# Optimization experiments

Hardware: AMD Instinct MI355X
Metric: run time of the kernel (lower is better)

Reference implementation:

```python
import jax, jax.numpy as jnp
import numpy as np

V = 25000
E = 100000
NODE_IN = 74
EDGE_IN = 12
OUT = 64
EHID = 128
NUM_STEPS = 6


def setup_inputs() -> dict:
    key = jax.random.key(0)
    ks = jax.random.split(key, 12)
    s = 0.05
    node_feats = jax.random.normal(ks[0], (V, NODE_IN), dtype=jnp.float32)
    edge_feats = jax.random.normal(ks[1], (E, EDGE_IN), dtype=jnp.float32)
    src = jax.random.randint(ks[2], (E,), 0, V)
    dst = jax.random.randint(ks[3], (E,), 0, V)
    # project_node_feats: Linear(node_in, out)
    Wp = jax.random.normal(ks[4], (NODE_IN, OUT), dtype=jnp.float32) * s
    bp = jnp.zeros((OUT,), dtype=jnp.float32)
    # edge network: Linear(edge_in, ehid) -> ReLU -> Linear(ehid, out*out)
    We1 = jax.random.normal(ks[5], (EDGE_IN, EHID), dtype=jnp.float32) * s
    be1 = jnp.zeros((EHID,), dtype=jnp.float32)
    We2 = jax.random.normal(ks[6], (EHID, OUT * OUT), dtype=jnp.float32) * s
    be2 = jnp.zeros((OUT * OUT,), dtype=jnp.float32)
    # NNConv output bias
    bias = jnp.zeros((OUT,), dtype=jnp.float32)
    return {
        "node_feats": node_feats, "edge_feats": edge_feats,
        "src": src, "dst": dst,
        "Wp": Wp, "bp": bp,
        "We1": We1, "be1": be1, "We2": We2, "be2": be2,
        "bias": bias,
    }


def reference(node_feats, edge_feats, src, dst, Wp, bp, We1, be1, We2, be2, bias):
    # project node features
    h = jax.nn.relu(node_feats @ Wp + bp)  # [V, OUT]
    # per-edge weight matrices (same every step -> hoist out of loop)
    ew = jax.nn.relu(edge_feats @ We1 + be1) @ We2 + be2  # [E, OUT*OUT]
    ew = ew.reshape(E, OUT, OUT)
    for _ in range(NUM_STEPS):
        # gather src node feats, batched matvec, scatter-sum to dst
        msg = jnp.einsum('ei,eio->eo', h[src], ew)  # [E, OUT]
        agg = jax.ops.segment_sum(msg, dst, num_segments=V)  # [V, OUT]
        h = jax.nn.relu(agg + bias)
    return h
```

## Files before the change

### kernel.cpp

```cpp
#include <hip/hip_runtime.h>
#include <hip/hip_bf16.h>

#define Vn 25000
#define En 100000
#define NODE_IN 74
#define EDGE_IN 12
#define OUTD 64
#define EHID 128
#define NUM_STEPS 6

#define HPAD 68

typedef __attribute__((ext_vector_type(8))) _Float16 half8;
typedef __attribute__((ext_vector_type(4))) float floatx4;

__global__ void proj_kernel(const float* __restrict__ node,
                            const float* __restrict__ Wp,
                            const float* __restrict__ bp,
                            float* __restrict__ h) {
  __shared__ float nf[NODE_IN];
  int v = blockIdx.x;
  int o = threadIdx.x;
  for (int i = o; i < NODE_IN; i += 64) nf[i] = node[(size_t)v * NODE_IN + i];
  __syncthreads();
  float acc = bp[o];
  for (int i = 0; i < NODE_IN; ++i) acc = fmaf(nf[i], Wp[i * OUTD + o], acc);
  h[(size_t)v * OUTD + o] = fmaxf(acc, 0.0f);
}

__global__ void edge_kernel(const float* __restrict__ ef,
                            const float* __restrict__ We1,
                            const float* __restrict__ be1,
                            _Float16* __restrict__ f) {
  __shared__ float es[EDGE_IN];
  int e = blockIdx.x;
  int k = threadIdx.x;
  if (k < EDGE_IN) es[k] = ef[(size_t)e * EDGE_IN + k];
  __syncthreads();
  float acc = be1[k];
  for (int j = 0; j < EDGE_IN; ++j) acc = fmaf(es[j], We1[j * EHID + k], acc);
  f[(size_t)e * EHID + k] = (_Float16)fmaxf(acc, 0.0f);
}

__global__ void w2r_kernel(const float* __restrict__ We2,
                           _Float16* __restrict__ w2s) {
  int g = blockIdx.x * 256 + threadIdx.x;
  int j = g & 7;
  int quad = (g >> 3) & 3;
  int l15 = (g >> 5) & 15;
  int c = (g >> 9) & 3;
  int step = g >> 11;
  int s = step & 3;
  int i = step >> 2;
  int k = s * 32 + quad * 8 + j;
  int col = i * 64 + c * 16 + l15;
  int eidx = g & 2047;
  int estore = eidx ^ (((eidx >> 6) & 3) << 3);
  w2s[((size_t)step << 11) | estore] = (_Float16)We2[(size_t)k * (OUTD * OUTD) + col];
}

#define GLOAD_LDS(gp, lp)                                                     \
  __builtin_amdgcn_global_load_lds(                                           \
      (const __attribute__((address_space(1))) void*)(gp),                    \
      (__attribute__((address_space(3))) void*)(lp), 16, 0, 0)

__global__ __launch_bounds__(256, 2) void msg_kernel(
    const float* __restrict__ h,
    const _Float16* __restrict__ f,
    const _Float16* __restrict__ w2s,
    const int* __restrict__ src,
    const int* __restrict__ dst,
    const float* __restrict__ be2,
    float* __restrict__ agg) {
  __shared__ __align__(16) char smem_raw[41472];
  __shared__ int s_dst[64];

  _Float16* h16 = (_Float16*)smem_raw;

  const int tid = threadIdx.x;
  const int wv = tid >> 6;
  const int lane = tid & 63;
  const int quad = lane >> 4;
  const int l15 = lane & 15;
  const int e0 = blockIdx.x * 64;

  if (tid < 64) {
    int e = e0 + tid;
    s_dst[tid] = (e < En) ? dst[e] : -1;
  }
  {
    int e = tid & 63;
    int ib = tid >> 6;
    int eg = e0 + e;
    int sv = (eg < En) ? src[eg] : 0;
    const float4* hp = reinterpret_cast<const float4*>(h + (size_t)sv * OUTD + ib * 16);
    for (int c = 0; c < 4; ++c) {
      float4 val = hp[c];
      int i4 = ib * 16 + c * 4;
      h16[(i4 + 0) * HPAD + e] = (_Float16)val.x;
      h16[(i4 + 1) * HPAD + e] = (_Float16)val.y;
      h16[(i4 + 2) * HPAD + e] = (_Float16)val.z;
      h16[(i4 + 3) * HPAD + e] = (_Float16)val.w;
    }
  }
  __syncthreads();

  half8 afr[4][4];
#pragma unroll
  for (int t = 0; t < 4; ++t) {
    int e = e0 + t * 16 + l15;
    if (e >= En) e = En - 1;
    const _Float16* fr = f + (size_t)e * EHID + quad * 8;
#pragma unroll
    for (int s = 0; s < 4; ++s)
      afr[t][s] = *reinterpret_cast<const half8*>(fr + s * 32);
  }

  floatx4 acc[4][4];
  const floatx4 zero4 = (floatx4){0.f, 0.f, 0.f, 0.f};
#pragma unroll
  for (int t = 0; t < 4; ++t)
#pragma unroll
    for (int c = 0; c < 4; ++c) acc[t][c] = zero4;

  const int ibase = wv * 16;

  char* ring = smem_raw + 8704 + wv * 8192;
  const char* w2b = (const char*)w2s;
  const int roff = l15 * 64 + ((quad ^ ((l15 >> 1) & 3)) << 4);
  const char* slot0p = ring + roff;
  const char* slot1p = ring + 4096 + roff;

#define STAGE(GS, SLOT)                                                       \
  {                                                                           \
    const char* gp_ = w2b + (size_t)(GS) * 4096 + lane * 16;                  \
    char* lp_ = ring + (SLOT) * 4096;                                         \
    GLOAD_LDS(gp_, lp_);                                                      \
    GLOAD_LDS(gp_ + 1024, lp_ + 1024);                                        \
    GLOAD_LDS(gp_ + 2048, lp_ + 2048);                                        \
    GLOAD_LDS(gp_ + 3072, lp_ + 3072);                                        \
  }

#define VM4 asm volatile("s_waitcnt vmcnt(4)" ::: "memory")
#define VM0 asm volatile("s_waitcnt vmcnt(0)" ::: "memory")
#define LGKM0 asm volatile("s_waitcnt lgkmcnt(0)" ::: "memory")
#define LGKM4 asm volatile("s_waitcnt lgkmcnt(4)" ::: "memory")
#define SB __builtin_amdgcn_sched_barrier(0)

#define KSTEP(SS, BCUR, BNXT, STSLOT, GST, LW, VW, DO_STAGE, DO_READ, RDP)    \
  {                                                                           \
    LW;                                                                       \
    SB;                                                                       \
    if (DO_STAGE) STAGE(GST, STSLOT);                                         \
    VW;                                                                       \
    if (DO_READ) {                                                            \
      BNXT[0] = *reinterpret_cast<const half8*>(RDP);                         \
      BNXT[1] = *reinterpret_cast<const half8*>(RDP + 1024);                  \
      BNXT[2] = *reinterpret_cast<const half8*>(RDP + 2048);                  \
      BNXT[3] = *reinterpret_cast<const half8*>(RDP + 3072);                  \
    }                                                                         \
    _Pragma("unroll") for (int t = 0; t < 4; ++t) {                           \
      half8 as = afr[t][SS] * hb[t];                                          \
      acc[t][0] = __builtin_amdgcn_mfma_f32_16x16x32_f16(as, BCUR[0], acc[t][0], 0, 0, 0); \
      acc[t][1] = __builtin_amdgcn_mfma_f32_16x16x32_f16(as, BCUR[1], acc[t][1], 0, 0, 0); \
      acc[t][2] = __builtin_amdgcn_mfma_f32_16x16x32_f16(as, BCUR[2], acc[t][2], 0, 0, 0); \
      acc[t][3] = __builtin_amdgcn_mfma_f32_16x16x32_f16(as, BCUR[3], acc[t][3], 0, 0, 0); \
    }                                                                         \
    SB;                                                                       \
  }

#define BUILD_HB(IV)                                                          \
  half8 hb[4];                                                                \
  _Pragma("unroll") for (int t = 0; t < 4; ++t) {                             \
    _Float16 hf = h16[(IV) * HPAD + t * 16 + l15];                            \
    hb[t] = (half8){hf, hf, hf, hf, hf, hf, hf, hf};                          \
  }

  STAGE(ibase * 4, 0);
  STAGE(ibase * 4 + 1, 1);
  VM4;
  half8 bE[4], bO[4];
  bE[0] = *reinterpret_cast<const half8*>(slot0p);
  bE[1] = *reinterpret_cast<const half8*>(slot0p + 1024);
  bE[2] = *reinterpret_cast<const half8*>(slot0p + 2048);
  bE[3] = *reinterpret_cast<const half8*>(slot0p + 3072);

  for (int ii = 0; ii < 15; ++ii) {
    int iv = ibase + ii;
    int gs = iv * 4;
    BUILD_HB(iv);
    KSTEP(0, bE, bO, 0, gs + 2, LGKM4, VM4, 1, 1, slot1p);
    KSTEP(1, bO, bE, 1, gs + 3, LGKM0, VM4, 1, 1, slot0p);
    KSTEP(2, bE, bO, 0, gs + 4, LGKM0, VM4, 1, 1, slot1p);
    KSTEP(3, bO, bE, 1, gs + 5, LGKM0, VM4, 1, 1, slot0p);
  }
  {
    int iv = ibase + 15;
    int gs = iv * 4;
    BUILD_HB(iv);
    KSTEP(0, bE, bO, 0, gs + 2, LGKM4, VM4, 1, 1, slot1p);
    KSTEP(1, bO, bE, 1, gs + 3, LGKM0, VM4, 1, 1, slot0p);
    KSTEP(2, bE, bO, 0, 0, LGKM0, VM0, 0, 1, slot1p);
    KSTEP(3, bO, bE, 1, 0, (void)0, (void)0, 0, 0, slot0p);
  }

  if (wv == 0) {
#pragma unroll
    for (int s = 0; s < 2; ++s) {
      half8 b2f[4];
#pragma unroll
      for (int c = 0; c < 4; ++c) {
        half8 v;
#pragma unroll
        for (int j = 0; j < 8; ++j)
          v[j] = (_Float16)be2[(s * 32 + quad * 8 + j) * 64 + c * 16 + l15];
        b2f[c] = v;
      }
#pragma unroll
      for (int t = 0; t < 4; ++t) {
        half8 ha;
#pragma unroll
        for (int j = 0; j < 8; ++j)
          ha[j] = h16[(s * 32 + quad * 8 + j) * HPAD + t * 16 + l15];
#pragma unroll
        for (int c = 0; c < 4; ++c)
          acc[t][c] = __builtin_amdgcn_mfma_f32_16x16x32_f16(ha, b2f[c], acc[t][c], 0, 0, 0);
      }
    }
  }

  floatx4* scv = reinterpret_cast<floatx4*>(smem_raw);

#define ST1(TG)                                                           \
  _Pragma("unroll") for (int c = 0; c < 4; ++c)                           \
      scv[wv * 512 + (((TG) & 1) * 4 + c) * 64 + lane] = acc[TG][c];
#define LD1(TK)                                                           \
  _Pragma("unroll") for (int c = 0; c < 4; ++c)                           \
      acc[TK][c] += scv[(wv ^ 1) * 512 + (((TK) & 1) * 4 + c) * 64 + lane];
#define ST2(TG)                                                           \
  _Pragma("unroll") for (int c = 0; c < 4; ++c)                           \
      scv[wv * 512 + c * 64 + lane] = acc[TG][c];
#define LD2(TK)                                                           \
  _Pragma("unroll") for (int c = 0; c < 4; ++c)                           \
      acc[TK][c] += scv[(wv ^ 2) * 512 + c * 64 + lane];
#define SCAT(TF)                                                          \
  {                                                                       \
    int rb = (TF) * 16 + quad * 4;                                        \
    _Pragma("unroll") for (int c = 0; c < 4; ++c) {                       \
      int col = c * 16 + l15;                                             \
      _Pragma("unroll") for (int r = 0; r < 4; ++r) {                     \
        int d = s_dst[rb + r];                                            \
        if (d >= 0) atomicAdd(&agg[(size_t)d * OUTD + col], acc[TF][c][r]); \
      }                                                                   \
    }                                                                     \
  }

  __syncthreads();
  if ((wv & 1) == 0) { ST1(2); ST1(3); } else { ST1(0); ST1(1); }
  __syncthreads();
  if ((wv & 1) == 0) { LD1(0); LD1(1); } else { LD1(2); LD1(3); }
  __syncthreads();
  if (wv == 0) { ST2(1); } else if (wv == 1) { ST2(3); }
  else if (wv == 2) { ST2(0); } else { ST2(2); }
  __syncthreads();
  if (wv == 0) { LD2(0); SCAT(0); }
  else if (wv == 1) { LD2(2); SCAT(2); }
  else if (wv == 2) { LD2(1); SCAT(1); }
  else { LD2(3); SCAT(3); }
}

__global__ void update_kernel(float* __restrict__ agg,
                              const float* __restrict__ bias,
                              float* __restrict__ hout,
                              float* __restrict__ dout, int last) {
  int g = blockIdx.x * 256 + threadIdx.x;
  if (g >= Vn * OUTD) return;
  float v = agg[g];
  agg[g] = 0.0f;
  float r = fmaxf(v + bias[g & 63], 0.0f);
  hout[g] = r;
  if (last) dout[g] = r;
}

extern "C" void kernel_launch(void* const* d_in, const int* in_sizes, int n_in,
                              void* d_out, int out_size, void* d_ws, size_t ws_size,
                              hipStream_t stream) {
  const float* node = (const float*)d_in[0];
  const float* edge = (const float*)d_in[1];
  const int* src = (const int*)d_in[2];
  const int* dst = (const int*)d_in[3];
  const float* Wp   = (const float*)d_in[4];
  const float* bp   = (const float*)d_in[5];
  const float* We1  = (const float*)d_in[6];
  const float* be1  = (const float*)d_in[7];
  const float* We2  = (const float*)d_in[8];
  const float* be2  = (const float*)d_in[9];
  const float* bias = (const float*)d_in[10];
  float* out = (float*)d_out;

  char* ws = (char*)d_ws;
  float* agg = (float*)(ws);
  float* h_a = (float*)(ws + 6400000);
  float* h_b = (float*)(ws + 12800000);
  _Float16* f   = (_Float16*)(ws + 19200000);
  _Float16* w2s = (_Float16*)(ws + 44800000);

  hipMemsetAsync(agg, 0, (size_t)Vn * OUTD * sizeof(float), stream);
  proj_kernel<<<Vn, 64, 0, stream>>>(node, Wp, bp, h_a);
  edge_kernel<<<En, 128, 0, stream>>>(edge, We1, be1, f);
  w2r_kernel<<<(OUTD * OUTD * EHID) / 256, 256, 0, stream>>>(We2, w2s);

  float* hin = h_a;
  float* hout = h_b;
  for (int s = 0; s < NUM_STEPS; ++s) {
    msg_kernel<<<(En + 63) / 64, 256, 0, stream>>>(hin, f, w2s, src, dst, be2, agg);
    update_kernel<<<(Vn * OUTD + 255) / 256, 256, 0, stream>>>(
        agg, bias, hout, out, s == NUM_STEPS - 1);
    float* t = hin; hin = hout; hout = t;
  }
}
```

Before: 839.2 us.

## Deepen W2 LDS staging ring to four slots with prefetched h vectors

The per-wave LDS ring for streaming We2 tiles grows from two to four 4KB slots, so three stages are in flight and each step waits with a looser vmcnt. The tail-special-case iteration is removed by clamping stage indices. The h16 tile is re-laid out so each lane reads its four edge values as one half4, and the next row is prefetched during the current step. s_setprio is raised around the MFMA block. LDS use grows to about 72KB per block, which may cut occupancy below the two blocks per CU that the launch bounds target.

After: 883.4 us. +5.3%, slower.

```diff
diff --git a/kernel.cpp b/kernel.cpp
--- a/kernel.cpp
+++ b/kernel.cpp
@@ -9,9 +9,8 @@
 #define EHID 128
 #define NUM_STEPS 6
 
-#define HPAD 68
-
 typedef __attribute__((ext_vector_type(8))) _Float16 half8;
+typedef __attribute__((ext_vector_type(4))) _Float16 half4;
 typedef __attribute__((ext_vector_type(4))) float floatx4;
 
 __global__ void proj_kernel(const float* __restrict__ node,
@@ -72,7 +71,7 @@
     const int* __restrict__ dst,
     const float* __restrict__ be2,
     float* __restrict__ agg) {
-  __shared__ __align__(16) char smem_raw[41472];
+  __shared__ __align__(16) char smem_raw[73728];
   __shared__ int s_dst[64];
 
   _Float16* h16 = (_Float16*)smem_raw;
@@ -94,13 +93,15 @@
     int eg = e0 + e;
     int sv = (eg < En) ? src[eg] : 0;
     const float4* hp = reinterpret_cast<const float4*>(h + (size_t)sv * OUTD + ib * 16);
+    int pe = (e & 15) * 4 + (e >> 4);
+#pragma unroll
     for (int c = 0; c < 4; ++c) {
-      float4 val = hp[c];
+      float4 v = hp[c];
       int i4 = ib * 16 + c * 4;
-      h16[(i4 + 0) * HPAD + e] = (_Float16)val.x;
-      h16[(i4 + 1) * HPAD + e] = (_Float16)val.y;
-      h16[(i4 + 2) * HPAD + e] = (_Float16)val.z;
-      h16[(i4 + 3) * HPAD + e] = (_Float16)val.w;
+      h16[(i4 + 0) * 64 + pe] = (_Float16)v.x;
+      h16[(i4 + 1) * 64 + pe] = (_Float16)v.y;
+      h16[(i4 + 2) * 64 + pe] = (_Float16)v.z;
+      h16[(i4 + 3) * 64 + pe] = (_Float16)v.w;
     }
   }
   __syncthreads();
@@ -115,6 +116,7 @@
     for (int s = 0; s < 4; ++s)
       afr[t][s] = *reinterpret_cast<const half8*>(fr + s * 32);
   }
+  asm volatile("s_waitcnt vmcnt(0)" ::: "memory");
 
   floatx4 acc[4][4];
   const floatx4 zero4 = (floatx4){0.f, 0.f, 0.f, 0.f};
@@ -124,12 +126,16 @@
     for (int c = 0; c < 4; ++c) acc[t][c] = zero4;
 
   const int ibase = wv * 16;
-
-  char* ring = smem_raw + 8704 + wv * 8192;
+  const int SBASE = ibase * 4;
+  const int SMAX = SBASE + 63;
+
+  char* ring = smem_raw + 8192 + wv * 16384;
   const char* w2b = (const char*)w2s;
   const int roff = l15 * 64 + ((quad ^ ((l15 >> 1) & 3)) << 4);
-  const char* slot0p = ring + roff;
-  const char* slot1p = ring + 4096 + roff;
+  const char* sp0 = ring + roff;
+  const char* sp1 = ring + 4096 + roff;
+  const char* sp2 = ring + 8192 + roff;
+  const char* sp3 = ring + 12288 + roff;
 
 #define STAGE(GS, SLOT)                                                       \
   {                                                                           \
@@ -141,68 +147,69 @@
     GLOAD_LDS(gp_ + 3072, lp_ + 3072);                                        \
   }
 
-#define VM4 asm volatile("s_waitcnt vmcnt(4)" ::: "memory")
+#define VM8 asm volatile("s_waitcnt vmcnt(8)" ::: "memory")
 #define VM0 asm volatile("s_waitcnt vmcnt(0)" ::: "memory")
 #define LGKM0 asm volatile("s_waitcnt lgkmcnt(0)" ::: "memory")
 #define LGKM4 asm volatile("s_waitcnt lgkmcnt(4)" ::: "memory")
+#define LGKM5 asm volatile("s_waitcnt lgkmcnt(5)" ::: "memory")
 #define SB __builtin_amdgcn_sched_barrier(0)
 
-#define KSTEP(SS, BCUR, BNXT, STSLOT, GST, LW, VW, DO_STAGE, DO_READ, RDP)    \
+#define KSTEP(SS, BMM, BRD, STSL, RDP, GST, LW)                               \
   {                                                                           \
     LW;                                                                       \
     SB;                                                                       \
-    if (DO_STAGE) STAGE(GST, STSLOT);                                         \
-    VW;                                                                       \
-    if (DO_READ) {                                                            \
-      BNXT[0] = *reinterpret_cast<const half8*>(RDP);                         \
-      BNXT[1] = *reinterpret_cast<const half8*>(RDP + 1024);                  \
-      BNXT[2] = *reinterpret_cast<const half8*>(RDP + 2048);                  \
-      BNXT[3] = *reinterpret_cast<const half8*>(RDP + 3072);                  \
-    }                                                                         \
+    int gs_ = (GST) > SMAX ? SMAX : (GST);                                    \
+    STAGE(gs_, STSL);                                                         \
+    VM8;                                                                      \
+    BRD[0] = *reinterpret_cast<const half8*>(RDP);                            \
+    BRD[1] = *reinterpret_cast<const half8*>(RDP + 1024);                     \
+    BRD[2] = *reinterpret_cast<const half8*>(RDP + 2048);                     \
+    BRD[3] = *reinterpret_cast<const half8*>(RDP + 3072);                     \
+    __builtin_amdgcn_s_setprio(1);                                            \
     _Pragma("unroll") for (int t = 0; t < 4; ++t) {                           \
       half8 as = afr[t][SS] * hb[t];                                          \
-      acc[t][0] = __builtin_amdgcn_mfma_f32_16x16x32_f16(as, BCUR[0], acc[t][0], 0, 0, 0); \
-      acc[t][1] = __builtin_amdgcn_mfma_f32_16x16x32_f16(as, BCUR[1], acc[t][1], 0, 0, 0); \
-      acc[t][2] = __builtin_amdgcn_mfma_f32_16x16x32_f16(as, BCUR[2], acc[t][2], 0, 0, 0); \
-      acc[t][3] = __builtin_amdgcn_mfma_f32_16x16x32_f16(as, BCUR[3], acc[t][3], 0, 0, 0); \
+      acc[t][0] = __builtin_amdgcn_mfma_f32_16x16x32_f16(as, BMM[0], acc[t][0], 0, 0, 0); \
+      acc[t][1] = __builtin_amdgcn_mfma_f32_16x16x32_f16(as, BMM[1], acc[t][1], 0, 0, 0); \
+      acc[t][2] = __builtin_amdgcn_mfma_f32_16x16x32_f16(as, BMM[2], acc[t][2], 0, 0, 0); \
+      acc[t][3] = __builtin_amdgcn_mfma_f32_16x16x32_f16(as, BMM[3], acc[t][3], 0, 0, 0); \
     }                                                                         \
-    SB;                                                                       \
-  }
-
-#define BUILD_HB(IV)                                                          \
-  half8 hb[4];                                                                \
-  _Pragma("unroll") for (int t = 0; t < 4; ++t) {                             \
-    _Float16 hf = h16[(IV) * HPAD + t * 16 + l15];                            \
-    hb[t] = (half8){hf, hf, hf, hf, hf, hf, hf, hf};                          \
-  }
-
-  STAGE(ibase * 4, 0);
-  STAGE(ibase * 4 + 1, 1);
-  VM4;
-  half8 bE[4], bO[4];
-  bE[0] = *reinterpret_cast<const half8*>(slot0p);
-  bE[1] = *reinterpret_cast<const half8*>(slot0p + 1024);
-  bE[2] = *reinterpret_cast<const half8*>(slot0p + 2048);
-  bE[3] = *reinterpret_cast<const half8*>(slot0p + 3072);
-
-  for (int ii = 0; ii < 15; ++ii) {
-    int iv = ibase + ii;
-    int gs = iv * 4;
-    BUILD_HB(iv);
-    KSTEP(0, bE, bO, 0, gs + 2, LGKM4, VM4, 1, 1, slot1p);
-    KSTEP(1, bO, bE, 1, gs + 3, LGKM0, VM4, 1, 1, slot0p);
-    KSTEP(2, bE, bO, 0, gs + 4, LGKM0, VM4, 1, 1, slot1p);
-    KSTEP(3, bO, bE, 1, gs + 5, LGKM0, VM4, 1, 1, slot0p);
-  }
-  {
-    int iv = ibase + 15;
-    int gs = iv * 4;
-    BUILD_HB(iv);
-    KSTEP(0, bE, bO, 0, gs + 2, LGKM4, VM4, 1, 1, slot1p);
-    KSTEP(1, bO, bE, 1, gs + 3, LGKM0, VM4, 1, 1, slot0p);
-    KSTEP(2, bE, bO, 0, 0, LGKM0, VM0, 0, 1, slot1p);
-    KSTEP(3, bO, bE, 1, 0, (void)0, (void)0, 0, 0, slot0p);
-  }
+    __builtin_amdgcn_s_setprio(0);                                            \
+  }
+
+  STAGE(SBASE, 0);
+  STAGE(SBASE + 1, 1);
+  STAGE(SBASE + 2, 2);
+  VM8;
+  half8 P[4], Q[4];
+  P[0] = *reinterpret_cast<const half8*>(sp0);
+  P[1] = *reinterpret_cast<const half8*>(sp0 + 1024);
+  P[2] = *reinterpret_cast<const half8*>(sp0 + 2048);
+  P[3] = *reinterpret_cast<const half8*>(sp0 + 3072);
+
+  half4 hv = *reinterpret_cast<const half4*>(h16 + ibase * 64 + l15 * 4);
+  half4 hvn;
+
+  for (int ii = 0; ii < 16; ++ii) {
+    half8 hb[4];
+#pragma unroll
+    for (int t = 0; t < 4; ++t) {
+      _Float16 hf = hv[t];
+      hb[t] = (half8){hf, hf, hf, hf, hf, hf, hf, hf};
+    }
+    int gs = SBASE + ii * 4;
+    KSTEP(0, P, Q, 3, sp1, gs + 3, LGKM4);
+    {
+      int inx = (ii < 15) ? ii + 1 : 15;
+      hvn = *reinterpret_cast<const half4*>(h16 + (ibase + inx) * 64 + l15 * 4);
+    }
+    KSTEP(1, Q, P, 0, sp2, gs + 4, LGKM5);
+    KSTEP(2, P, Q, 1, sp3, gs + 5, LGKM4);
+    KSTEP(3, Q, P, 2, sp0, gs + 6, LGKM4);
+    hv = hvn;
+  }
+
+  VM0;
+  LGKM0;
 
   if (wv == 0) {
 #pragma unroll
@@ -221,7 +228,7 @@
         half8 ha;
 #pragma unroll
         for (int j = 0; j < 8; ++j)
-          ha[j] = h16[(s * 32 + quad * 8 + j) * HPAD + t * 16 + l15];
+          ha[j] = h16[(s * 32 + quad * 8 + j) * 64 + l15 * 4 + t];
 #pragma unroll
         for (int c = 0; c < 4; ++c)
           acc[t][c] = __builtin_amdgcn_mfma_f32_16x16x32_f16(ha, b2f[c], acc[t][c], 0, 0, 0);
```
